# Optimization experiments

Measured on AMD Instinct MI355X. Metric: run time of the kernel, lower is better.

## Reference

```python
import jax, jax.numpy as jnp
import numpy as np

DIM = 1024

def setup_inputs() -> dict:
    key = jax.random.key(0)
    k1, k2 = jax.random.split(key)
    X = jax.random.normal(k1, (4, 4096, DIM), dtype=jnp.float32)
    # nn.Linear(dim, 3*dim): weight [3*dim, dim], bias [3*dim]
    W = jax.random.normal(k2, (3 * DIM, DIM), dtype=jnp.float32) * (1.0 / np.sqrt(DIM))
    b = jnp.zeros((3 * DIM,), dtype=jnp.float32)
    return {"X": X, "W": W, "b": b}

def reference(X, W, b):
    dim = X.shape[-1]
    # fused QKV projection: [B,S,3D]
    QKV = jnp.einsum('bsd,ed->bse', X, W) + b
    Q, K, V = jnp.split(QKV, 3, axis=-1)
    scale = 1.0 / jnp.sqrt(jnp.asarray(dim, X.dtype))
    scores = jnp.einsum('bqd,bkd->bqk', Q, K) * scale  # [B,S,S]
    attn = jax.nn.softmax(scores, axis=-1)
    return jnp.einsum('bqk,bkd->bqd', attn, V)
```

## Files before the change

### kernel.cpp

```cpp
#include <hip/hip_runtime.h>
#include <cstdint>

typedef unsigned short u16;
typedef __attribute__((ext_vector_type(8))) short bf16x8;
typedef __attribute__((ext_vector_type(4))) float f32x4;

#define DIM   1024
#define BATCH 4
#define SEQ   4096
#define E3    3072
#define MTOT  (BATCH*SEQ)

__device__ __forceinline__ u16 f2bf(float x) {
    union { float f; unsigned u; } v; v.f = x;
    unsigned r = v.u + 0x7FFFu + ((v.u >> 16) & 1u);
    return (u16)(r >> 16);
}

__device__ __forceinline__ void gl16(const void* g, void* l) {
    __builtin_amdgcn_global_load_lds(
        (const __attribute__((address_space(1))) void*)g,
        (__attribute__((address_space(3))) void*)l, 16, 0, 0);
}

__device__ __forceinline__ void gemm256(
    const u16* __restrict__ A, int sA,
    const u16* __restrict__ B, int sB,
    int K, int m0, int n0,
    u16* lds, f32x4 acc[8][4])
{
    const int t   = threadIdx.x;
    const int w   = t >> 6, L = t & 63;
    const int rL  = L & 15, kq = L >> 4;
    const int qa  = 2*w;
    const int ia0 = 8*(w>>2);
    const int jb0 = 4*(w&3);

    const size_t ga0 = (size_t)(m0 + qa*16 + rL)*sA + kq*8;
    const size_t ga1 = ga0 + (size_t)16*sA;
    const size_t gb0 = (size_t)(n0 + qa*16 + rL)*sB + kq*8;
    const size_t gb1 = gb0 + (size_t)16*sB;

    const int NT = K >> 5;
    bf16x8 av[8], bv[4];

#define STAGE_A(tile) { const size_t k0=(size_t)(tile)*32; \
    u16* sb = lds + ((tile)&3)*16384; \
    gl16(A + ga0 + k0, sb + qa*512); \
    gl16(A + ga1 + k0, sb + qa*512 + 512); }
#define STAGE_B(tile) { const size_t k0=(size_t)(tile)*32; \
    u16* sb = lds + ((tile)&3)*16384; \
    gl16(B + gb0 + k0, sb + 8192 + qa*512); \
    gl16(B + gb1 + k0, sb + 8192 + qa*512 + 512); }

#define MEMB  asm volatile("" ::: "memory")
#define BAR   __builtin_amdgcn_s_barrier()
#define LGKM0 asm volatile("s_waitcnt lgkmcnt(0)" ::: "memory")
#define VM(n) asm volatile("s_waitcnt vmcnt(" #n ")" ::: "memory")

#define PH0(tile, DOSTAGE) { \
    const u16* sb = lds + ((tile)&3)*16384; \
    _Pragma("unroll") \
    for (int i = 0; i < 4; ++i) av[i] = *(const bf16x8*)&sb[(ia0+i)*512 + L*8]; \
    _Pragma("unroll") \
    for (int j = 0; j < 4; ++j) bv[j] = *(const bf16x8*)&sb[8192 + (jb0+j)*512 + L*8]; \
    if (DOSTAGE) STAGE_A((tile)+3); \
    MEMB; BAR; LGKM0; \
    __builtin_amdgcn_s_setprio(1); \
    _Pragma("unroll") \
    for (int i = 0; i < 4; ++i) \
        _Pragma("unroll") \
        for (int j = 0; j < 4; ++j) \
            acc[i][j] = __builtin_amdgcn_mfma_f32_16x16x32_bf16(av[i], bv[j], acc[i][j], 0,0,0); \
    __builtin_amdgcn_s_setprio(0); \
    MEMB; BAR; }

#define PH1(tile, DOSTAGE, WAIT) { \
    const u16* sb = lds + ((tile)&3)*16384; \
    _Pragma("unroll") \
    for (int i = 0; i < 4; ++i) av[4+i] = *(const bf16x8*)&sb[(ia0+4+i)*512 + L*8]; \
    if (DOSTAGE) STAGE_B((tile)+3); \
    MEMB; BAR; LGKM0; \
    __builtin_amdgcn_s_setprio(1); \
    _Pragma("unroll") \
    for (int i = 0; i < 4; ++i) \
        _Pragma("unroll") \
        for (int j = 0; j < 4; ++j) \
            acc[4+i][j] = __builtin_amdgcn_mfma_f32_16x16x32_bf16(av[4+i], bv[j], acc[4+i][j], 0,0,0); \
    __builtin_amdgcn_s_setprio(0); \
    WAIT; MEMB; BAR; }

    STAGE_A(0); STAGE_B(0);
    STAGE_A(1); STAGE_B(1);
    STAGE_A(2); STAGE_B(2);
    VM(8); BAR;

    for (int tt = 0; tt < NT-3; ++tt) {
        PH0(tt, 1);
        PH1(tt, 1, VM(8));
    }
    PH0(NT-3, 0); PH1(NT-3, 0, VM(4));
    PH0(NT-2, 0); PH1(NT-2, 0, VM(0));
    PH0(NT-1, 0); PH1(NT-1, 0, (void)0);

#undef STAGE_A
#undef STAGE_B
#undef PH0
#undef PH1
#undef MEMB
#undef BAR
#undef LGKM0
#undef VM
}

__global__ __launch_bounds__(256)
void cvt_bf16(const float* __restrict__ x, u16* __restrict__ y) {
    size_t i = ((size_t)blockIdx.x*256 + threadIdx.x)*4;
    float4 v = *(const float4*)&x[i];
    ushort4 h;
    h.x = f2bf(v.x); h.y = f2bf(v.y); h.z = f2bf(v.z); h.w = f2bf(v.w);
    *(ushort4*)&y[i] = h;
}

__global__ __launch_bounds__(512,2)
void gemm_qkv(const u16* __restrict__ Xbf, const u16* __restrict__ Wbf,
              const float* __restrict__ bias,
              u16* __restrict__ Qh, u16* __restrict__ Kh,
              u16* __restrict__ Vth)
{
    __shared__ __align__(16) u16 lds[65536];
    f32x4 acc[8][4];
    #pragma unroll
    for (int i=0;i<8;++i)
        #pragma unroll
        for (int j=0;j<4;++j) acc[i][j] = (f32x4){0.f,0.f,0.f,0.f};

    const int m0 = blockIdx.y*256, n0 = blockIdx.x*256;
    gemm256(Xbf, DIM, Wbf, DIM, DIM, m0, n0, lds, acc);

    const int t = threadIdx.x, w = t>>6, L = t&63;
    const int wm = 128*(w>>2), wn = 64*(w&3);
    const int cl = L&15, rq = (L>>4)*4;
    const int region = n0 >> 10;
    const float qscale = 0.03125f;

    if (region < 2) {
        u16* Dst = region ? Kh : Qh;
        const float fs = region ? 1.0f : qscale;
        #pragma unroll
        for (int j = 0; j < 4; ++j) {
            float bc = bias[n0 + wn + j*16 + cl];
            #pragma unroll
            for (int i = 0; i < 8; ++i)
                #pragma unroll
                for (int r = 0; r < 4; ++r)
                    acc[i][j][r] = (acc[i][j][r] + bc)*fs;
        }
        const int d0 = (n0 & 1023) + wn;
        #pragma unroll
        for (int p = 0; p < 2; ++p) {
            const int nt0 = 2*p, nt1 = 2*p+1;
            #pragma unroll
            for (int i = 0; i < 8; ++i) {
                int row0 = m0 + wm + i*16 + rq;
                int bi = row0 >> 12, s0 = row0 & (SEQ-1);
                #pragma unroll
                for (int r = 0; r < 4; ++r) {
                    float v0 = acc[i][nt0][r], v1 = acc[i][nt1][r];
                    float x0 = __shfl_xor(v0, 1, 64);
                    float x1 = __shfl_xor(v1, 1, 64);
                    unsigned wv; int colb;
                    if ((cl & 1) == 0) {
                        wv   = (unsigned)f2bf(v0) | ((unsigned)f2bf(x0) << 16);
                        colb = nt0*16 + cl;
                    } else {
                        wv   = (unsigned)f2bf(x1) | ((unsigned)f2bf(v1) << 16);
                        colb = nt1*16 + (cl-1);
                    }
                    size_t idx = ((size_t)bi*SEQ + s0 + r)*DIM + d0 + colb;
                    *(unsigned*)&Dst[idx] = wv;
                }
            }
        }
    } else {
        #pragma unroll
        for (int j = 0; j < 4; ++j) {
            int col = n0 + wn + j*16 + cl;
            float bc = bias[col];
            int d = col & (DIM-1);
            #pragma unroll
            for (int i = 0; i < 8; ++i) {
                int row0 = m0 + wm + i*16 + rq;
                int bi = row0 >> 12, s0 = row0 & (SEQ-1);
                ushort4 hv;
                hv.x = f2bf(acc[i][j][0] + bc);
                hv.y = f2bf(acc[i][j][1] + bc);
                hv.z = f2bf(acc[i][j][2] + bc);
                hv.w = f2bf(acc[i][j][3] + bc);
                size_t base = ((size_t)bi*DIM + d)*SEQ + s0;
                *(ushort4*)&Vth[base] = hv;
            }
        }
    }
}

__global__ __launch_bounds__(512,2)
void gemm_scores(const u16* __restrict__ Qh, const u16* __restrict__ Kh,
                 u16* __restrict__ S0, u16* __restrict__ S1,
                 u16* __restrict__ S2, u16* __restrict__ S3)
{
    __shared__ __align__(16) u16 lds[65536];
    f32x4 acc[8][4];
    #pragma unroll
    for (int i=0;i<8;++i)
        #pragma unroll
        for (int j=0;j<4;++j) acc[i][j] = (f32x4){0.f,0.f,0.f,0.f};

    const int bz = blockIdx.z;
    const size_t qo = (size_t)bz*SEQ*DIM;
    const int m0 = blockIdx.y*256, n0 = blockIdx.x*256;
    gemm256(Qh + qo, DIM, Kh + qo, DIM, DIM, m0, n0, lds, acc);

    u16* Sb = (bz == 0) ? S0 : (bz == 1) ? S1 : (bz == 2) ? S2 : S3;
    const int t = threadIdx.x, w = t>>6, L = t&63;
    const int wm = 128*(w>>2), wn = 64*(w&3);
    const int cl = L&15, rq = (L>>4)*4;
    #pragma unroll
    for (int p = 0; p < 2; ++p) {
        const int nt0 = 2*p, nt1 = 2*p+1;
        #pragma unroll
        for (int i = 0; i < 8; ++i) {
            int row0 = m0 + wm + i*16 + rq;
            #pragma unroll
            for (int r = 0; r < 4; ++r) {
                float v0 = acc[i][nt0][r], v1 = acc[i][nt1][r];
                float x0 = __shfl_xor(v0, 1, 64);
                float x1 = __shfl_xor(v1, 1, 64);
                unsigned wv; int colb;
                if ((cl & 1) == 0) {
                    wv   = (unsigned)f2bf(v0) | ((unsigned)f2bf(x0) << 16);
                    colb = nt0*16 + cl;
                } else {
                    wv   = (unsigned)f2bf(x1) | ((unsigned)f2bf(v1) << 16);
                    colb = nt1*16 + (cl-1);
                }
                *(unsigned*)&Sb[(size_t)(row0 + r)*SEQ + n0 + wn + colb] = wv;
            }
        }
    }
}

__global__ __launch_bounds__(256)
void softmax_pack(u16* __restrict__ S0, u16* __restrict__ S1,
                  u16* __restrict__ S2, u16* __restrict__ S3)
{
    __shared__ float red[4];
    const int t = threadIdx.x, L = t & 63, w = t >> 6;
    const int gr = blockIdx.x, bz = gr >> 12, rr = gr & (SEQ-1);
    u16* Sb = (bz == 0) ? S0 : (bz == 1) ? S1 : (bz == 2) ? S2 : S3;
    u16* row = Sb + (size_t)rr*SEQ;

    float v[16];
    float m = -1e30f;
    #pragma unroll
    for (int j = 0; j < 2; ++j) {
        ushort4 x0 = *(const ushort4*)&row[t*8 + j*2048];
        ushort4 x1 = *(const ushort4*)&row[t*8 + j*2048 + 4];
        union { unsigned u; float f; } c;
        c.u = (unsigned)x0.x << 16; v[8*j+0] = c.f;
        c.u = (unsigned)x0.y << 16; v[8*j+1] = c.f;
        c.u = (unsigned)x0.z << 16; v[8*j+2] = c.f;
        c.u = (unsigned)x0.w << 16; v[8*j+3] = c.f;
        c.u = (unsigned)x1.x << 16; v[8*j+4] = c.f;
        c.u = (unsigned)x1.y << 16; v[8*j+5] = c.f;
        c.u = (unsigned)x1.z << 16; v[8*j+6] = c.f;
        c.u = (unsigned)x1.w << 16; v[8*j+7] = c.f;
    }
    #pragma unroll
    for (int i = 0; i < 16; ++i) m = fmaxf(m, v[i]);
    #pragma unroll
    for (int off = 32; off; off >>= 1) m = fmaxf(m, __shfl_xor(m, off, 64));
    if (L == 0) red[w] = m;
    __syncthreads();
    m = fmaxf(fmaxf(red[0],red[1]), fmaxf(red[2],red[3]));

    float s = 0.f;
    #pragma unroll
    for (int i = 0; i < 16; ++i) { v[i] = __expf(v[i] - m); s += v[i]; }
    #pragma unroll
    for (int off = 32; off; off >>= 1) s += __shfl_xor(s, off, 64);
    __syncthreads();
    if (L == 0) red[w] = s;
    __syncthreads();
    s = red[0]+red[1]+red[2]+red[3];
    const float inv = 1.0f / s;

    #pragma unroll
    for (int j = 0; j < 2; ++j) {
        ushort4 h0, h1;
        h0.x = f2bf(v[8*j+0]*inv); h0.y = f2bf(v[8*j+1]*inv);
        h0.z = f2bf(v[8*j+2]*inv); h0.w = f2bf(v[8*j+3]*inv);
        h1.x = f2bf(v[8*j+4]*inv); h1.y = f2bf(v[8*j+5]*inv);
        h1.z = f2bf(v[8*j+6]*inv); h1.w = f2bf(v[8*j+7]*inv);
        *(ushort4*)&row[t*8 + j*2048]     = h0;
        *(ushort4*)&row[t*8 + j*2048 + 4] = h1;
    }
}

__global__ __launch_bounds__(512,2)
void gemm_pv(const u16* __restrict__ P0, const u16* __restrict__ P1,
             const u16* __restrict__ P2, const u16* __restrict__ P3,
             const u16* __restrict__ Vth,
             float* __restrict__ O0, float* __restrict__ O1,
             float* __restrict__ O2, float* __restrict__ O3)
{
    __shared__ __align__(16) u16 lds[65536];
    f32x4 acc[8][4];
    #pragma unroll
    for (int i=0;i<8;++i)
        #pragma unroll
        for (int j=0;j<4;++j) acc[i][j] = (f32x4){0.f,0.f,0.f,0.f};

    const int bz = blockIdx.z;
    const u16* Pb = (bz == 0) ? P0 : (bz == 1) ? P1 : (bz == 2) ? P2 : P3;
    float*     Ob = (bz == 0) ? O0 : (bz == 1) ? O1 : (bz == 2) ? O2 : O3;
    const int m0 = blockIdx.y*256, n0 = blockIdx.x*256;
    gemm256(Pb, SEQ, Vth + (size_t)bz*DIM*SEQ, SEQ, SEQ, m0, n0, lds, acc);

    const int t = threadIdx.x, w = t>>6, L = t&63;
    const int wm = 128*(w>>2), wn = 64*(w&3);
    const int cl = L&15, rq = (L>>4)*4;
    #pragma unroll
    for (int j = 0; j < 4; ++j) {
        int col = n0 + wn + j*16 + cl;
        #pragma unroll
        for (int i = 0; i < 8; ++i) {
            int row0 = m0 + wm + i*16 + rq;
            #pragma unroll
            for (int r = 0; r < 4; ++r)
                Ob[(size_t)(row0 + r)*DIM + col] = acc[i][j][r];
        }
    }
}

__global__ __launch_bounds__(256)
void copy_out(const float* __restrict__ src, float* __restrict__ dst)
{
    size_t i = ((size_t)blockIdx.x*256 + threadIdx.x)*4;
    *(float4*)&dst[i] = *(const float4*)&src[i];
}

extern "C" void kernel_launch(void* const* d_in, const int* in_sizes, int n_in,
                              void* d_out, int out_size, void* d_ws, size_t ws_size,
                              hipStream_t stream) {
    const float* X    = (const float*)d_in[0];
    const float* W    = (const float*)d_in[1];
    const float* bias = (const float*)d_in[2];
    float* out = (float*)d_out;

    const size_t MB = (size_t)1 << 20;
    if (ws_size < 192*MB) return;
    char* ws = (char*)d_ws;
    char* wo = (char*)d_out;
    u16* Qh  = (u16*)ws;
    u16* Kh  = (u16*)(ws + 32*MB);
    u16* Vth = (u16*)(ws + 64*MB);
    u16* S0  = (u16*)(ws + 96*MB);
    u16* S1  = (u16*)(ws + 128*MB);
    u16* S2  = (u16*)(ws + 160*MB);
    u16* Xbf = (u16*)wo;
    u16* Wbf = (u16*)(wo + 32*MB);
    u16* S3  = (u16*)(wo + 32*MB);
    float* O0 = (float*)wo;
    float* O1 = (float*)(wo + 16*MB);
    float* O2 = (float*)ws;
    float* O3 = (float*)(ws + 16*MB);

    cvt_bf16<<<MTOT*DIM/1024, 256, 0, stream>>>(X, Xbf);
    cvt_bf16<<<E3*DIM/1024,   256, 0, stream>>>(W, Wbf);

    gemm_qkv<<<dim3(E3/256, MTOT/256), 512, 0, stream>>>(
        Xbf, Wbf, bias, Qh, Kh, Vth);

    gemm_scores<<<dim3(SEQ/256, SEQ/256, BATCH), 512, 0, stream>>>(
        Qh, Kh, S0, S1, S2, S3);

    softmax_pack<<<MTOT, 256, 0, stream>>>(S0, S1, S2, S3);

    gemm_pv<<<dim3(DIM/256, SEQ/256, BATCH), 512, 0, stream>>>(
        S0, S1, S2, S3, Vth, O0, O1, O2, O3);

    copy_out<<<(32*MB/sizeof(float))/1024, 256, 0, stream>>>(
        (const float*)ws, out + 8*MB);
}
```

Baseline: 615.4 us.

## Software-pipeline LDS fragment reads one tile ahead in QKV GEMM mainloop

Restructures the GEMM mainloop so the A and B fragments for the next k-tile are read from LDS during the current tile's MFMA phase. This uses double-buffered B registers (even/odd) and split A registers. The explicit lgkmcnt(0) wait and one barrier per phase are removed, so LDS read latency can hide behind the MFMAs. In exchange it raises register pressure and changes the vmcnt accounting and loop unrolling, which risks spills at the 512x2 launch bound and subtle hazards in buffer reuse.

```diff
diff --git a/kernel.cpp b/kernel.cpp
--- a/kernel.cpp
+++ b/kernel.cpp
@@ -42,7 +42,7 @@
     const size_t gb1 = gb0 + (size_t)16*sB;
 
     const int NT = K >> 5;
-    bf16x8 av[8], bv[4];
+    bf16x8 av0[4], av1[4], bvE[4], bvO[4];
 
 #define STAGE_A(tile) { const size_t k0=(size_t)(tile)*32; \
     u16* sb = lds + ((tile)&3)*16384; \
@@ -55,62 +55,72 @@
 
 #define MEMB  asm volatile("" ::: "memory")
 #define BAR   __builtin_amdgcn_s_barrier()
-#define LGKM0 asm volatile("s_waitcnt lgkmcnt(0)" ::: "memory")
 #define VM(n) asm volatile("s_waitcnt vmcnt(" #n ")" ::: "memory")
-
-#define PH0(tile, DOSTAGE) { \
+#define NOP   ((void)0)
+
+#define PHA(tile, BV, DOSTAGE, PUBWAIT) { \
     const u16* sb = lds + ((tile)&3)*16384; \
     _Pragma("unroll") \
-    for (int i = 0; i < 4; ++i) av[i] = *(const bf16x8*)&sb[(ia0+i)*512 + L*8]; \
-    _Pragma("unroll") \
-    for (int j = 0; j < 4; ++j) bv[j] = *(const bf16x8*)&sb[8192 + (jb0+j)*512 + L*8]; \
+    for (int i = 0; i < 4; ++i) av1[i] = *(const bf16x8*)&sb[(ia0+4+i)*512 + L*8]; \
     if (DOSTAGE) STAGE_A((tile)+3); \
-    MEMB; BAR; LGKM0; \
+    MEMB; \
     __builtin_amdgcn_s_setprio(1); \
     _Pragma("unroll") \
     for (int i = 0; i < 4; ++i) \
         _Pragma("unroll") \
         for (int j = 0; j < 4; ++j) \
-            acc[i][j] = __builtin_amdgcn_mfma_f32_16x16x32_bf16(av[i], bv[j], acc[i][j], 0,0,0); \
+            acc[i][j] = __builtin_amdgcn_mfma_f32_16x16x32_bf16(av0[i], BV[j], acc[i][j], 0,0,0); \
     __builtin_amdgcn_s_setprio(0); \
-    MEMB; BAR; }
-
-#define PH1(tile, DOSTAGE, WAIT) { \
-    const u16* sb = lds + ((tile)&3)*16384; \
-    _Pragma("unroll") \
-    for (int i = 0; i < 4; ++i) av[4+i] = *(const bf16x8*)&sb[(ia0+4+i)*512 + L*8]; \
+    PUBWAIT; MEMB; BAR; }
+
+#define PHB(tile, BV_CUR, BV_NXT, DOSTAGE, DOREAD) { \
+    const u16* sbn = lds + (((tile)+1)&3)*16384; \
+    if (DOREAD) { \
+        _Pragma("unroll") \
+        for (int i = 0; i < 4; ++i) av0[i] = *(const bf16x8*)&sbn[(ia0+i)*512 + L*8]; \
+        _Pragma("unroll") \
+        for (int j = 0; j < 4; ++j) BV_NXT[j] = *(const bf16x8*)&sbn[8192 + (jb0+j)*512 + L*8]; \
+    } \
     if (DOSTAGE) STAGE_B((tile)+3); \
-    MEMB; BAR; LGKM0; \
+    MEMB; \
     __builtin_amdgcn_s_setprio(1); \
     _Pragma("unroll") \
     for (int i = 0; i < 4; ++i) \
         _Pragma("unroll") \
         for (int j = 0; j < 4; ++j) \
-            acc[4+i][j] = __builtin_amdgcn_mfma_f32_16x16x32_bf16(av[4+i], bv[j], acc[4+i][j], 0,0,0); \
+            acc[4+i][j] = __builtin_amdgcn_mfma_f32_16x16x32_bf16(av1[i], BV_CUR[j], acc[4+i][j], 0,0,0); \
     __builtin_amdgcn_s_setprio(0); \
-    WAIT; MEMB; BAR; }
+    MEMB; BAR; }
 
     STAGE_A(0); STAGE_B(0);
     STAGE_A(1); STAGE_B(1);
     STAGE_A(2); STAGE_B(2);
     VM(8); BAR;
-
-    for (int tt = 0; tt < NT-3; ++tt) {
-        PH0(tt, 1);
-        PH1(tt, 1, VM(8));
-    }
-    PH0(NT-3, 0); PH1(NT-3, 0, VM(4));
-    PH0(NT-2, 0); PH1(NT-2, 0, VM(0));
-    PH0(NT-1, 0); PH1(NT-1, 0, (void)0);
+    {
+        const u16* sb = lds;
+        #pragma unroll
+        for (int i = 0; i < 4; ++i) av0[i] = *(const bf16x8*)&sb[(ia0+i)*512 + L*8];
+        #pragma unroll
+        for (int j = 0; j < 4; ++j) bvE[j] = *(const bf16x8*)&sb[8192 + (jb0+j)*512 + L*8];
+    }
+
+    for (int tt = 0; tt < NT-4; tt += 2) {
+        PHA(tt,   bvE, 1, VM(6));  PHB(tt,   bvE, bvO, 1, 1);
+        PHA(tt+1, bvO, 1, VM(6));  PHB(tt+1, bvO, bvE, 1, 1);
+    }
+    PHA(NT-4, bvE, 1, VM(6));  PHB(NT-4, bvE, bvO, 1, 1);
+    PHA(NT-3, bvO, 0, VM(4));  PHB(NT-3, bvO, bvE, 0, 1);
+    PHA(NT-2, bvE, 0, VM(0));  PHB(NT-2, bvE, bvO, 0, 1);
+    PHA(NT-1, bvO, 0, NOP);    PHB(NT-1, bvO, bvE, 0, 0);
 
 #undef STAGE_A
 #undef STAGE_B
-#undef PH0
-#undef PH1
+#undef PHA
+#undef PHB
 #undef MEMB
 #undef BAR
-#undef LGKM0
 #undef VM
+#undef NOP
 }
 
 __global__ __launch_bounds__(256)
```

Result: no change. 612.9 us (-0.4%).
